# Performance work log

Hardware: AMD Instinct MI355X
Metric: run time of the kernel (lower is better)

Reference implementation:

```python
import jax, jax.numpy as jnp
import numpy as np

N_NODES = 100000
N_EDGES = 800000
IN_DIM, HID_DIM, OUT_DIM = 128, 256, 128


def setup_inputs() -> dict:
    key = jax.random.key(0)
    k1, k2, k3, k4, k5 = jax.random.split(key, 5)
    x = jax.random.normal(k1, (N_NODES, IN_DIM), dtype=jnp.float32)
    edge_index = jax.random.randint(k2, (2, N_EDGES), 0, N_NODES, dtype=jnp.int64)
    edge_weight = jax.random.uniform(k3, (N_EDGES,), dtype=jnp.float32)
    W1 = jax.random.normal(k4, (IN_DIM, HID_DIM), dtype=jnp.float32) * 0.02
    b1 = jnp.zeros((HID_DIM,), dtype=jnp.float32)
    W2 = jax.random.normal(k5, (HID_DIM, OUT_DIM), dtype=jnp.float32) * 0.02
    b2 = jnp.zeros((OUT_DIM,), dtype=jnp.float32)
    return {"x": x, "edge_index": edge_index, "edge_weight": edge_weight,
            "W1": W1, "b1": b1, "W2": W2, "b2": b2}


def reference(x, edge_index, edge_weight, W1, b1, W2, b2):
    # GCNConv (normalize=True, add_self_loops=False), two layers with ReLU.
    # Dropout is identity at inference.
    row = edge_index[0]  # source nodes (E,)
    col = edge_index[1]  # target nodes (E,)
    n = x.shape[0]

    # Symmetric normalization: deg at target, norm = d^-1/2[row]*w*d^-1/2[col]
    deg = jax.ops.segment_sum(edge_weight, col, num_segments=n)  # (N,)
    dis = jnp.where(deg > 0, jax.lax.rsqrt(deg), 0.0)
    norm = dis[row] * edge_weight * dis[col]  # (E,)

    def gcn_conv(h, W, b):
        h = h @ W                                   # (N, F_out)
        msg = h[row] * norm[:, None]                # (E, F_out) gather+scale
        agg = jax.ops.segment_sum(msg, col, num_segments=n)  # scatter-add
        return agg + b

    h = jax.nn.relu(gcn_conv(x.astype(jnp.float32), W1, b1))
    return gcn_conv(h, W2, b2)
```

## Files before the change

kernel.cpp:

```cpp
#include <hip/hip_runtime.h>
#include <hip/hip_bf16.h>
#include <cstdint>
#include <cstddef>

#define N_NODES 100000
#define N_EDGES 800000
#define IN_DIM 128
#define HID_DIM 256
#define OUT_DIM 128

typedef __attribute__((ext_vector_type(8))) short bf16x8;
typedef __attribute__((ext_vector_type(4))) float f32x4;

__device__ __forceinline__ unsigned short f32_to_bf16(float f) {
    __hip_bfloat16 b = __float2bfloat16(f);
    return *reinterpret_cast<unsigned short*>(&b);
}
__device__ __forceinline__ float bf16_lo(uint32_t u) {
    uint32_t v = u << 16; return *reinterpret_cast<float*>(&v);
}
__device__ __forceinline__ float bf16_hi(uint32_t u) {
    uint32_t v = u & 0xffff0000u; return *reinterpret_cast<float*>(&v);
}

__global__ void rank_hist_kernel(const int* __restrict__ ei,
                                 int* __restrict__ cnt,
                                 int* __restrict__ rank) {
    int e = blockIdx.x * 256 + threadIdx.x;
    if (e >= N_EDGES) return;
    rank[e] = atomicAdd(&cnt[ei[N_EDGES + e]], 1);
}

__global__ void scan1_kernel(const int* __restrict__ in, int* __restrict__ out,
                             int* __restrict__ bsums, int n) {
    __shared__ int tmp[256];
    int t = threadIdx.x;
    int i = blockIdx.x * 256 + t;
    int v = (i < n) ? in[i] : 0;
    tmp[t] = v;
    __syncthreads();
    for (int off = 1; off < 256; off <<= 1) {
        int u = (t >= off) ? tmp[t - off] : 0;
        __syncthreads();
        tmp[t] += u;
        __syncthreads();
    }
    if (i < n) out[i] = tmp[t] - v;
    if (t == 255) bsums[blockIdx.x] = tmp[255];
}

__global__ void scan2_kernel(int* __restrict__ bsums, int nb) {
    __shared__ int tmp[512];
    int t = threadIdx.x;
    int v = (t < nb) ? bsums[t] : 0;
    tmp[t] = v;
    __syncthreads();
    for (int off = 1; off < 512; off <<= 1) {
        int u = (t >= off) ? tmp[t - off] : 0;
        __syncthreads();
        tmp[t] += u;
        __syncthreads();
    }
    if (t < nb) bsums[t] = tmp[t] - v;
}

__global__ void scan3_kernel(int* __restrict__ rowp, const int* __restrict__ bsums,
                             int n, int total) {
    int i = blockIdx.x * 256 + threadIdx.x;
    if (i == 0) rowp[n] = total;
    if (i >= n) return;
    rowp[i] += bsums[blockIdx.x];
}

__global__ void place_kernel(const int* __restrict__ ei,
                             const float* __restrict__ ew,
                             const int* __restrict__ rank,
                             const int* __restrict__ rowp,
                             int2* __restrict__ pairs) {
    int e = blockIdx.x * 256 + threadIdx.x;
    if (e >= N_EDGES) return;
    int c = ei[N_EDGES + e];
    int pos = rowp[c] + rank[e];
    pairs[pos] = make_int2(ei[e], __float_as_int(ew[e]));
}

__global__ void deg_dis_kernel(const int* __restrict__ rowp,
                               const int2* __restrict__ pairs,
                               float* __restrict__ dis) {
    int v = blockIdx.x * 256 + threadIdx.x;
    if (v >= N_NODES) return;
    int b = rowp[v], e = rowp[v + 1];
    float d = 0.f;
    for (int j = b; j < e; ++j) d += __int_as_float(pairs[j].y);
    dis[v] = d > 0.f ? rsqrtf(d) : 0.f;
}

__global__ void prep_kernel(const float* __restrict__ x, uint32_t* __restrict__ xb,
                            const float* __restrict__ W1, unsigned short* __restrict__ W1F,
                            const float* __restrict__ W2, unsigned short* __restrict__ W2F) {
    int b = blockIdx.x;
    if (b < 12500) {
        int i = b * 256 + threadIdx.x;
        float4 v = ((const float4*)x)[i];
        uint32_t lo = (uint32_t)f32_to_bf16(v.x) | ((uint32_t)f32_to_bf16(v.y) << 16);
        uint32_t hi = (uint32_t)f32_to_bf16(v.z) | ((uint32_t)f32_to_bf16(v.w) << 16);
        ((uint2*)xb)[i] = make_uint2(lo, hi);
    } else if (b < 12628) {
        int idx = (b - 12500) * 256 + threadIdx.x;
        int j = idx & 7, lane = (idx >> 3) & 63;
        int nt = (idx >> 9) & 3, ks = (idx >> 11) & 3;
        int wc = (idx >> 13) & 1, nh = (idx >> 14) & 1;
        int fr = lane & 15, fq = lane >> 4;
        int row = nh * 128 + wc * 64 + nt * 16 + fr;
        int kk = ks * 32 + fq * 8 + j;
        W1F[idx] = f32_to_bf16(W1[kk * HID_DIM + row]);
    } else {
        int idx = (b - 12628) * 256 + threadIdx.x;
        int j = idx & 7, lane = (idx >> 3) & 63;
        int nt = (idx >> 9) & 3, ks = (idx >> 11) & 3;
        int wc = (idx >> 13) & 1, nh = (idx >> 14) & 1;
        int fr = lane & 15, fq = lane >> 4;
        int n = wc * 64 + nt * 16 + fr;
        int kk = nh * 128 + ks * 32 + fq * 8 + j;
        W2F[idx] = f32_to_bf16(W2[kk * OUT_DIM + n]);
    }
}

template <bool OUT_BF16>
__global__ void aggregate_kernel(const uint2* __restrict__ feat,
                                 const int* __restrict__ rowp,
                                 const int2* __restrict__ pairs,
                                 const float* __restrict__ dis,
                                 void* __restrict__ out_v,
                                 const float* __restrict__ bias) {
    int gtid = blockIdx.x * blockDim.x + threadIdx.x;
    int node = gtid >> 5;
    int lane = threadIdx.x & 31;
    if (node >= N_NODES) return;
    int beg = rowp[node], end = rowp[node + 1];
    float dv = dis[node];
    float ax = 0.f, ay = 0.f, az = 0.f, aw = 0.f;

    int j = beg;
    for (; j + 4 <= end; j += 4) {
        int2 p[4]; uint2 u[4]; float d[4];
        #pragma unroll
        for (int q = 0; q < 4; ++q) p[q] = pairs[j + q];
        #pragma unroll
        for (int q = 0; q < 4; ++q) {
            u[q] = feat[(size_t)p[q].x * 32 + lane];
            d[q] = dis[p[q].x];
        }
        #pragma unroll
        for (int q = 0; q < 4; ++q) {
            float w = __int_as_float(p[q].y) * d[q] * dv;
            ax += w * bf16_lo(u[q].x); ay += w * bf16_hi(u[q].x);
            az += w * bf16_lo(u[q].y); aw += w * bf16_hi(u[q].y);
        }
    }
    if (j + 2 <= end) {
        int2 p0 = pairs[j], p1 = pairs[j + 1];
        uint2 u0 = feat[(size_t)p0.x * 32 + lane];
        uint2 u1 = feat[(size_t)p1.x * 32 + lane];
        float w0 = __int_as_float(p0.y) * dis[p0.x] * dv;
        float w1 = __int_as_float(p1.y) * dis[p1.x] * dv;
        ax += w0 * bf16_lo(u0.x) + w1 * bf16_lo(u1.x);
        ay += w0 * bf16_hi(u0.x) + w1 * bf16_hi(u1.x);
        az += w0 * bf16_lo(u0.y) + w1 * bf16_lo(u1.y);
        aw += w0 * bf16_hi(u0.y) + w1 * bf16_hi(u1.y);
        j += 2;
    }
    if (j < end) {
        int2 p0 = pairs[j];
        uint2 u0 = feat[(size_t)p0.x * 32 + lane];
        float w0 = __int_as_float(p0.y) * dis[p0.x] * dv;
        ax += w0 * bf16_lo(u0.x); ay += w0 * bf16_hi(u0.x);
        az += w0 * bf16_lo(u0.y); aw += w0 * bf16_hi(u0.y);
    }
    if (bias) {
        float4 b = ((const float4*)bias)[lane];
        ax += b.x; ay += b.y; az += b.z; aw += b.w;
    }
    if (OUT_BF16) {
        uint2 o;
        o.x = (uint32_t)f32_to_bf16(ax) | ((uint32_t)f32_to_bf16(ay) << 16);
        o.y = (uint32_t)f32_to_bf16(az) | ((uint32_t)f32_to_bf16(aw) << 16);
        ((uint2*)out_v)[(size_t)node * 32 + lane] = o;
    } else {
        ((float4*)out_v)[(size_t)node * 32 + lane] = make_float4(ax, ay, az, aw);
    }
}

__global__ __launch_bounds__(256, 2) void gemm_fused_kernel(
    const unsigned short* __restrict__ A,
    const unsigned short* __restrict__ W1F,
    const float* __restrict__ b1,
    const unsigned short* __restrict__ W2F,
    unsigned short* __restrict__ T,
    int M) {
    __shared__ unsigned short As[128 * 128];
    __shared__ unsigned short Hs[128 * 136];
    int tid = threadIdx.x;
    int wave = tid >> 6, lane = tid & 63;
    int m0 = blockIdx.x * 128;
    int wr = (wave & 1) * 64;
    int wcid = wave >> 1;
    int wc = wcid * 64;
    int fr = lane & 15, fq = lane >> 4;

    #pragma unroll
    for (int i = 0; i < 8; ++i) {
        int cbase = (i * 4 + wave) * 64;
        int c = cbase + lane;
        int m = c >> 4, cl = c & 15;
        int qg = ((cl & 7) ^ (m & 7)) | (cl & 8);
        int gm = m0 + m; if (gm >= M) gm = M - 1;
        const unsigned short* ga = A + (size_t)gm * 128 + qg * 8;
        __builtin_amdgcn_global_load_lds(
            (const __attribute__((address_space(1))) void*)ga,
            (__attribute__((address_space(3))) void*)(As + (size_t)cbase * 8),
            16, 0, 0);
    }
    __syncthreads();

    bf16x8 af[4][4];
    #pragma unroll
    for (int ks = 0; ks < 4; ++ks) {
        int q = ks * 4 + fq;
        int cl = ((q & 7) ^ (fr & 7)) | (q & 8);
        #pragma unroll
        for (int mt = 0; mt < 4; ++mt)
            af[ks][mt] = *(const bf16x8*)(As + (wr + mt * 16 + fr) * 128 + cl * 8);
    }

    const bf16x8* w1p = (const bf16x8*)W1F;
    const bf16x8* w2p = (const bf16x8*)W2F;

    f32x4 acc_t[4][4] = {};
    #pragma unroll
    for (int nh = 0; nh < 2; ++nh) {
        int wbase = (nh * 2 + wcid) * 16 * 64;
        f32x4 acc_h[4][4] = {};
        #pragma unroll
        for (int ks = 0; ks < 4; ++ks) {
            bf16x8 wf[4];
            #pragma unroll
            for (int nt = 0; nt < 4; ++nt)
                wf[nt] = w1p[wbase + (ks * 4 + nt) * 64 + lane];
            #pragma unroll
            for (int mt = 0; mt < 4; ++mt)
                #pragma unroll
                for (int nt = 0; nt < 4; ++nt)
                    acc_h[mt][nt] = __builtin_amdgcn_mfma_f32_16x16x32_bf16(
                        af[ks][mt], wf[nt], acc_h[mt][nt], 0, 0, 0);
        }
        float bv[4];
        #pragma unroll
        for (int nt = 0; nt < 4; ++nt) bv[nt] = b1[nh * 128 + wc + nt * 16 + fr];
        __syncthreads();
        #pragma unroll
        for (int mt = 0; mt < 4; ++mt)
            #pragma unroll
            for (int r = 0; r < 4; ++r) {
                int row = wr + mt * 16 + fq * 4 + r;
                #pragma unroll
                for (int nt = 0; nt < 4; ++nt) {
                    float v = fmaxf(acc_h[mt][nt][r] + bv[nt], 0.f);
                    Hs[row * 136 + wc + nt * 16 + fr] = f32_to_bf16(v);
                }
            }
        __syncthreads();
        #pragma unroll
        for (int ks = 0; ks < 4; ++ks) {
            bf16x8 wf[4], hf[4];
            #pragma unroll
            for (int nt = 0; nt < 4; ++nt)
                wf[nt] = w2p[wbase + (ks * 4 + nt) * 64 + lane];
            #pragma unroll
            for (int mt = 0; mt < 4; ++mt)
                hf[mt] = *(const bf16x8*)(Hs + (wr + mt * 16 + fr) * 136 + ks * 32 + fq * 8);
            #pragma unroll
            for (int mt = 0; mt < 4; ++mt)
                #pragma unroll
                for (int nt = 0; nt < 4; ++nt)
                    acc_t[mt][nt] = __builtin_amdgcn_mfma_f32_16x16x32_bf16(
                        hf[mt], wf[nt], acc_t[mt][nt], 0, 0, 0);
        }
    }

    #pragma unroll
    for (int mt = 0; mt < 4; ++mt)
        #pragma unroll
        for (int r = 0; r < 4; ++r) {
            int row = m0 + wr + mt * 16 + fq * 4 + r;
            if (row >= M) continue;
            #pragma unroll
            for (int nt = 0; nt < 4; ++nt)
                T[(size_t)row * 128 + wc + nt * 16 + fr] = f32_to_bf16(acc_t[mt][nt][r]);
        }
}

extern "C" void kernel_launch(void* const* d_in, const int* in_sizes, int n_in,
                              void* d_out, int out_size, void* d_ws, size_t ws_size,
                              hipStream_t stream) {
    const float* x  = (const float*)d_in[0];
    const int*   ei = (const int*)d_in[1];
    const float* ew = (const float*)d_in[2];
    const float* W1 = (const float*)d_in[3];
    const float* b1 = (const float*)d_in[4];
    const float* W2 = (const float*)d_in[5];
    const float* b2 = (const float*)d_in[6];
    float* out = (float*)d_out;

    char* ws = (char*)d_ws;
    size_t off = 0;
    auto alloc = [&](size_t bytes) -> void* {
        void* p = ws + off;
        off = (off + bytes + 255) & ~(size_t)255;
        return p;
    };
    int*   cnt   = (int*)  alloc((size_t)N_NODES * 4);
    float* dis   = (float*)alloc((size_t)N_NODES * 4);
    int*   rowp  = (int*)  alloc((size_t)(N_NODES + 1) * 4);
    int*   bsums = (int*)  alloc(512 * 4);
    int*   rank  = (int*)  alloc((size_t)N_EDGES * 4);
    int2*  pairs = (int2*) alloc((size_t)N_EDGES * 8);
    uint32_t* xb = (uint32_t*)alloc((size_t)N_NODES * IN_DIM * 2);
    unsigned short* W1F = (unsigned short*)alloc((size_t)IN_DIM * HID_DIM * 2);
    unsigned short* W2F = (unsigned short*)alloc((size_t)HID_DIM * OUT_DIM * 2);
    unsigned short* A1  = (unsigned short*)alloc((size_t)N_NODES * IN_DIM * 2);
    unsigned short* t   = (unsigned short*)alloc((size_t)N_NODES * OUT_DIM * 2);

    hipMemsetAsync(cnt, 0, (size_t)N_NODES * 4, stream);

    int ne_blocks = (N_EDGES + 255) / 256;
    int nn_blocks = (N_NODES + 255) / 256;

    rank_hist_kernel<<<ne_blocks, 256, 0, stream>>>(ei, cnt, rank);
    scan1_kernel<<<nn_blocks, 256, 0, stream>>>(cnt, rowp, bsums, N_NODES);
    scan2_kernel<<<1, 512, 0, stream>>>(bsums, nn_blocks);
    scan3_kernel<<<nn_blocks, 256, 0, stream>>>(rowp, bsums, N_NODES, N_EDGES);
    place_kernel<<<ne_blocks, 256, 0, stream>>>(ei, ew, rank, rowp, pairs);
    deg_dis_kernel<<<nn_blocks, 256, 0, stream>>>(rowp, pairs, dis);
    prep_kernel<<<12756, 256, 0, stream>>>(x, xb, W1, W1F, W2, W2F);

    int agg_blocks = (N_NODES * 32) / 256;

    aggregate_kernel<true><<<agg_blocks, 256, 0, stream>>>(
        (const uint2*)xb, rowp, pairs, dis, A1, nullptr);

    gemm_fused_kernel<<<(N_NODES + 127) / 128, 256, 0, stream>>>(
        A1, W1F, b1, W2F, t, N_NODES);

    aggregate_kernel<false><<<agg_blocks, 256, 0, stream>>>(
        (const uint2*)t, rowp, pairs, dis, out, b2);
}
```

Measured before the change: 279.9 us.

## Precompute normalized edge weights, fuse degree into histogram, widen aggregate lanes

Degree is now accumulated with float atomics during the histogram pass, and dis is computed in the scan fixup, which removes the separate deg_dis kernel. The place kernel stores the fully normalized edge weight, so the aggregate kernels no longer gather dis per edge. Each aggregation row is now handled by 16 lanes loading 16 bytes each instead of 32 lanes loading 8 bytes. Float atomic accumulation makes the degree sum order nondeterministic, and the wider per-thread loads raise register use.

```diff
diff --git a/kernel.cpp b/kernel.cpp
--- a/kernel.cpp
+++ b/kernel.cpp
@@ -24,11 +24,15 @@
 }
 
 __global__ void rank_hist_kernel(const int* __restrict__ ei,
+                                 const float* __restrict__ ew,
                                  int* __restrict__ cnt,
+                                 float* __restrict__ deg,
                                  int* __restrict__ rank) {
     int e = blockIdx.x * 256 + threadIdx.x;
     if (e >= N_EDGES) return;
-    rank[e] = atomicAdd(&cnt[ei[N_EDGES + e]], 1);
+    int c = ei[N_EDGES + e];
+    rank[e] = atomicAdd(&cnt[c], 1);
+    atomicAdd(&deg[c], ew[e]);
 }
 
 __global__ void scan1_kernel(const int* __restrict__ in, int* __restrict__ out,
@@ -65,34 +69,29 @@
 }
 
 __global__ void scan3_kernel(int* __restrict__ rowp, const int* __restrict__ bsums,
+                             const float* __restrict__ deg, float* __restrict__ dis,
                              int n, int total) {
     int i = blockIdx.x * 256 + threadIdx.x;
     if (i == 0) rowp[n] = total;
     if (i >= n) return;
     rowp[i] += bsums[blockIdx.x];
+    float d = deg[i];
+    dis[i] = d > 0.f ? rsqrtf(d) : 0.f;
 }
 
 __global__ void place_kernel(const int* __restrict__ ei,
                              const float* __restrict__ ew,
                              const int* __restrict__ rank,
                              const int* __restrict__ rowp,
+                             const float* __restrict__ dis,
                              int2* __restrict__ pairs) {
     int e = blockIdx.x * 256 + threadIdx.x;
     if (e >= N_EDGES) return;
+    int s = ei[e];
     int c = ei[N_EDGES + e];
     int pos = rowp[c] + rank[e];
-    pairs[pos] = make_int2(ei[e], __float_as_int(ew[e]));
-}
-
-__global__ void deg_dis_kernel(const int* __restrict__ rowp,
-                               const int2* __restrict__ pairs,
-                               float* __restrict__ dis) {
-    int v = blockIdx.x * 256 + threadIdx.x;
-    if (v >= N_NODES) return;
-    int b = rowp[v], e = rowp[v + 1];
-    float d = 0.f;
-    for (int j = b; j < e; ++j) d += __int_as_float(pairs[j].y);
-    dis[v] = d > 0.f ? rsqrtf(d) : 0.f;
+    float wn = ew[e] * dis[s] * dis[c];
+    pairs[pos] = make_int2(s, __float_as_int(wn));
 }
 
 __global__ void prep_kernel(const float* __restrict__ x, uint32_t* __restrict__ xb,
@@ -126,68 +125,67 @@
     }
 }
 
+__device__ __forceinline__ void acc_edge(float w, uint4 u, float* a) {
+    a[0] += w * bf16_lo(u.x); a[1] += w * bf16_hi(u.x);
+    a[2] += w * bf16_lo(u.y); a[3] += w * bf16_hi(u.y);
+    a[4] += w * bf16_lo(u.z); a[5] += w * bf16_hi(u.z);
+    a[6] += w * bf16_lo(u.w); a[7] += w * bf16_hi(u.w);
+}
+
 template <bool OUT_BF16>
-__global__ void aggregate_kernel(const uint2* __restrict__ feat,
+__global__ void aggregate_kernel(const uint4* __restrict__ feat,
                                  const int* __restrict__ rowp,
                                  const int2* __restrict__ pairs,
-                                 const float* __restrict__ dis,
                                  void* __restrict__ out_v,
                                  const float* __restrict__ bias) {
     int gtid = blockIdx.x * blockDim.x + threadIdx.x;
-    int node = gtid >> 5;
-    int lane = threadIdx.x & 31;
+    int node = gtid >> 4;
+    int lane = threadIdx.x & 15;
     if (node >= N_NODES) return;
     int beg = rowp[node], end = rowp[node + 1];
-    float dv = dis[node];
-    float ax = 0.f, ay = 0.f, az = 0.f, aw = 0.f;
+    float a[8] = {};
 
     int j = beg;
     for (; j + 4 <= end; j += 4) {
-        int2 p[4]; uint2 u[4]; float d[4];
+        int2 p[4]; uint4 u[4];
         #pragma unroll
         for (int q = 0; q < 4; ++q) p[q] = pairs[j + q];
         #pragma unroll
-        for (int q = 0; q < 4; ++q) {
-            u[q] = feat[(size_t)p[q].x * 32 + lane];
-            d[q] = dis[p[q].x];
-        }
-        #pragma unroll
-        for (int q = 0; q < 4; ++q) {
-            float w = __int_as_float(p[q].y) * d[q] * dv;
-            ax += w * bf16_lo(u[q].x); ay += w * bf16_hi(u[q].x);
-            az += w * bf16_lo(u[q].y); aw += w * bf16_hi(u[q].y);
-        }
+        for (int q = 0; q < 4; ++q) u[q] = feat[(size_t)p[q].x * 16 + lane];
+        #pragma unroll
+        for (int q = 0; q < 4; ++q) acc_edge(__int_as_float(p[q].y), u[q], a);
     }
     if (j + 2 <= end) {
         int2 p0 = pairs[j], p1 = pairs[j + 1];
-        uint2 u0 = feat[(size_t)p0.x * 32 + lane];
-        uint2 u1 = feat[(size_t)p1.x * 32 + lane];
-        float w0 = __int_as_float(p0.y) * dis[p0.x] * dv;
-        float w1 = __int_as_float(p1.y) * dis[p1.x] * dv;
-        ax += w0 * bf16_lo(u0.x) + w1 * bf16_lo(u1.x);
-        ay += w0 * bf16_hi(u0.x) + w1 * bf16_hi(u1.x);
-        az += w0 * bf16_lo(u0.y) + w1 * bf16_lo(u1.y);
-        aw += w0 * bf16_hi(u0.y) + w1 * bf16_hi(u1.y);
+        uint4 u0 = feat[(size_t)p0.x * 16 + lane];
+        uint4 u1 = feat[(size_t)p1.x * 16 + lane];
+        acc_edge(__int_as_float(p0.y), u0, a);
+        acc_edge(__int_as_float(p1.y), u1, a);
         j += 2;
     }
     if (j < end) {
         int2 p0 = pairs[j];
-        uint2 u0 = feat[(size_t)p0.x * 32 + lane];
-        float w0 = __int_as_float(p0.y) * dis[p0.x] * dv;
-        ax += w0 * bf16_lo(u0.x); ay += w0 * bf16_hi(u0.x);
-        az += w0 * bf16_lo(u0.y); aw += w0 * bf16_hi(u0.y);
+        uint4 u0 = feat[(size_t)p0.x * 16 + lane];
+        acc_edge(__int_as_float(p0.y), u0, a);
     }
     if (bias) {
-        float4 b = ((const float4*)bias)[lane];
-        ax += b.x; ay += b.y; az += b.z; aw += b.w;
+        float4 b0 = ((const float4*)bias)[lane * 2];
+        float4 b1 = ((const float4*)bias)[lane * 2 + 1];
+        a[0] += b0.x; a[1] += b0.y; a[2] += b0.z; a[3] += b0.w;
+        a[4] += b1.x; a[5] += b1.y; a[6] += b1.z; a[7] += b1.w;
     }
     if (OUT_BF16) {
-        uint2 o;
-        o.x = (uint32_t)f32_to_bf16(ax) | ((uint32_t)f32_to_bf16(ay) << 16);
-        o.y = (uint32_t)f32_to_bf16(az) | ((uint32_t)f32_to_bf16(aw) << 16);
-        ((uint2*)out_v)[(size_t)node * 32 + lane] = o;
+        uint4 o;
+        o.x = (uint32_t)f32_to_bf16(a[0]) | ((uint32_t)f32_to_bf16(a[1]) << 16);
+        o.y = (uint32_t)f32_to_bf16(a[2]) | ((uint32_t)f32_to_bf16(a[3]) << 16);
+        o.z = (uint32_t)f32_to_bf16(a[4]) | ((uint32_t)f32_to_bf16(a[5]) << 16);
+        o.w = (uint32_t)f32_to_bf16(a[6]) | ((uint32_t)f32_to_bf16(a[7]) << 16);
+        ((uint4*)out_v)[(size_t)node * 16 + lane] = o;
     } else {
-        ((float4*)out_v)[(size_t)node * 32 + lane] = make_float4(ax, ay, az, aw);
+        ((float4*)out_v)[(size_t)node * 32 + lane * 2] =
+            make_float4(a[0], a[1], a[2], a[3]);
+        ((float4*)out_v)[(size_t)node * 32 + lane * 2 + 1] =
+            make_float4(a[4], a[5], a[6], a[7]);
     }
 }
 
@@ -319,7 +317,8 @@
         off = (off + bytes + 255) & ~(size_t)255;
         return p;
     };
-    int*   cnt   = (int*)  alloc((size_t)N_NODES * 4);
+    int*   cnt   = (int*)  alloc((size_t)N_NODES * 8);
+    float* deg   = (float*)(cnt + N_NODES);
     float* dis   = (float*)alloc((size_t)N_NODES * 4);
     int*   rowp  = (int*)  alloc((size_t)(N_NODES + 1) * 4);
     int*   bsums = (int*)  alloc(512 * 4);
@@ -331,27 +330,26 @@
     unsigned short* A1  = (unsigned short*)alloc((size_t)N_NODES * IN_DIM * 2);
     unsigned short* t   = (unsigned short*)alloc((size_t)N_NODES * OUT_DIM * 2);
 
-    hipMemsetAsync(cnt, 0, (size_t)N_NODES * 4, stream);
+    hipMemsetAsync(cnt, 0, (size_t)N_NODES * 8, stream);
 
     int ne_blocks = (N_EDGES + 255) / 256;
     int nn_blocks = (N_NODES + 255) / 256;
 
-    rank_hist_kernel<<<ne_blocks, 256, 0, stream>>>(ei, cnt, rank);
+    rank_hist_kernel<<<ne_blocks, 256, 0, stream>>>(ei, ew, cnt, deg, rank);
     scan1_kernel<<<nn_blocks, 256, 0, stream>>>(cnt, rowp, bsums, N_NODES);
     scan2_kernel<<<1, 512, 0, stream>>>(bsums, nn_blocks);
-    scan3_kernel<<<nn_blocks, 256, 0, stream>>>(rowp, bsums, N_NODES, N_EDGES);
-    place_kernel<<<ne_blocks, 256, 0, stream>>>(ei, ew, rank, rowp, pairs);
-    deg_dis_kernel<<<nn_blocks, 256, 0, stream>>>(rowp, pairs, dis);
+    scan3_kernel<<<nn_blocks, 256, 0, stream>>>(rowp, bsums, deg, dis, N_NODES, N_EDGES);
+    place_kernel<<<ne_blocks, 256, 0, stream>>>(ei, ew, rank, rowp, dis, pairs);
     prep_kernel<<<12756, 256, 0, stream>>>(x, xb, W1, W1F, W2, W2F);
 
-    int agg_blocks = (N_NODES * 32) / 256;
+    int agg_blocks = (N_NODES * 16) / 256;
 
     aggregate_kernel<true><<<agg_blocks, 256, 0, stream>>>(
-        (const uint2*)xb, rowp, pairs, dis, A1, nullptr);
+        (const uint4*)xb, rowp, pairs, A1, nullptr);
 
     gemm_fused_kernel<<<(N_NODES + 127) / 128, 256, 0, stream>>>(
         A1, W1F, b1, W2F, t, N_NODES);
 
     aggregate_kernel<false><<<agg_blocks, 256, 0, stream>>>(
-        (const uint2*)t, rowp, pairs, dis, out, b2);
-}
+        (const uint4*)t, rowp, pairs, out, b2);
+}
```

Result: slower. 309.8 us (+10.7%).
